# Kernel tuning notes

Measured on AMD Instinct MI355X. Metric: run time of the kernel, lower is better.

The kernel has to match this reference:

```python
import jax, jax.numpy as jnp
import numpy as np
from jax import lax

T, B = 128, 32
V, H = 50257, 512


def _leaky(x, beta):
    # StateLeaky leaky integrator: mem[t] = beta * mem[t-1] + x[t], mem[-1] = 0.
    # x: [T, B, H], beta: [H] (broadcast per-channel decay)
    def step(mem, xt):
        mem = beta * mem + xt
        return mem, mem
    _, mem = lax.scan(step, jnp.zeros_like(x[0]), x)
    return mem  # [T, B, H]


def setup_inputs() -> dict:
    key = jax.random.key(0)
    ks = jax.random.split(key, 10)
    s_emb = 1.0  # nn.Embedding default init N(0,1)
    lim = 1.0 / np.sqrt(H)  # nn.Linear default U(-1/sqrt(fan_in), 1/sqrt(fan_in))
    return {
        "x": jax.random.randint(ks[0], (T, B), 0, V, dtype=jnp.int64),
        "emb": jax.random.normal(ks[1], (V, H), jnp.float32) * s_emb,
        "pos_emb": jax.random.normal(ks[2], (T, H), jnp.float32) * s_emb,
        "beta1": jnp.full((H,), 0.9, jnp.float32),
        "beta2": jnp.full((H,), 0.9, jnp.float32),
        "beta3": jnp.full((H,), 0.9, jnp.float32),
        "fc2_w": jax.random.uniform(ks[3], (H, H), jnp.float32, -lim, lim),
        "fc2_b": jax.random.uniform(ks[4], (H,), jnp.float32, -lim, lim),
        "fc3_w": jax.random.uniform(ks[5], (H, H), jnp.float32, -lim, lim),
        "fc3_b": jax.random.uniform(ks[6], (H,), jnp.float32, -lim, lim),
        "fco_w": jax.random.uniform(ks[7], (V, H), jnp.float32, -lim, lim),
        "fco_b": jax.random.uniform(ks[8], (V,), jnp.float32, -lim, lim),
    }


def reference(x, emb, pos_emb, beta1, beta2, beta3, fc2_w, fc2_b, fc3_w, fc3_b, fco_w, fco_b):
    # token embed + positional embed (pos broadcast over batch dim)
    h = emb[x] + pos_emb[:, None, :]                      # [T, B, H]
    h = _leaky(h, beta1)                                  # StateLeaky 1
    h = jax.nn.relu(jnp.einsum('tbh,oh->tbo', h, fc2_w) + fc2_b)
    h = _leaky(h, beta2)                                  # StateLeaky 2
    h = jax.nn.relu(jnp.einsum('tbh,oh->tbo', h, fc3_w) + fc3_b)
    h = _leaky(h, beta3)                                  # StateLeaky 3
    out = jnp.einsum('tbh,vh->tbv', h, fco_w) + fco_b     # [T, B, V] logits
    return out
```

## Files before the change

### kernel.cpp

```cpp
#include <hip/hip_runtime.h>

typedef __attribute__((ext_vector_type(8))) short short8;
typedef __attribute__((ext_vector_type(4))) float f32x4;
typedef unsigned short u16;
typedef unsigned int u32;

#define DEVI __device__ __forceinline__

DEVI u16 f2bf(float f) {
    union { float f; u32 u; } v; v.f = f;
    u32 r = v.u + 0x7FFFu + ((v.u >> 16) & 1u);
    return (u16)(r >> 16);
}

__global__ void cvt_bf16_kernel(const float* __restrict__ in, u16* __restrict__ out, int n4) {
    int i = blockIdx.x * blockDim.x + threadIdx.x;
    int stride = gridDim.x * blockDim.x;
    for (; i < n4; i += stride) {
        float4 v = reinterpret_cast<const float4*>(in)[i];
        ushort4 o;
        o.x = f2bf(v.x); o.y = f2bf(v.y); o.z = f2bf(v.z); o.w = f2bf(v.w);
        reinterpret_cast<ushort4*>(out)[i] = o;
    }
}

__global__ __launch_bounds__(64)
void embed_leaky_kernel(const int* __restrict__ x, const float* __restrict__ emb,
                        const float* __restrict__ pos, const float* __restrict__ beta,
                        u16* __restrict__ Aout) {
    __shared__ int xs[128];
    int gtid = blockIdx.x * 64 + threadIdx.x;
    int b = gtid >> 9;
    int h = gtid & 511;
    for (int i = threadIdx.x; i < 128; i += 64) xs[i] = x[i * 32 + b];
    __syncthreads();
    float be = beta[h];
    float mem = 0.f;
    for (int t0 = 0; t0 < 128; t0 += 8) {
        float e[8];
#pragma unroll
        for (int j = 0; j < 8; ++j)
            e[j] = emb[(size_t)xs[t0 + j] * 512 + h] + pos[(t0 + j) * 512 + h];
#pragma unroll
        for (int j = 0; j < 8; ++j) {
            mem = be * mem + e[j];
            Aout[(size_t)((t0 + j) * 32 + b) * 512 + h] = f2bf(mem);
        }
    }
}

__global__ __launch_bounds__(64)
void leaky_bf16_kernel(const float* __restrict__ in, const float* __restrict__ beta,
                       u16* __restrict__ Aout) {
    int gtid = blockIdx.x * 64 + threadIdx.x;
    int b = gtid >> 9;
    int h = gtid & 511;
    float be = beta[h];
    float mem = 0.f;
    for (int t0 = 0; t0 < 128; t0 += 8) {
        float v[8];
#pragma unroll
        for (int j = 0; j < 8; ++j)
            v[j] = in[(size_t)((t0 + j) * 32 + b) * 512 + h];
#pragma unroll
        for (int j = 0; j < 8; ++j) {
            mem = be * mem + v[j];
            Aout[(size_t)((t0 + j) * 32 + b) * 512 + h] = f2bf(mem);
        }
    }
}

template<bool RELU>
__global__ __launch_bounds__(256)
void gemm_bt_128(const u16* __restrict__ A, const u16* __restrict__ B,
                 const float* __restrict__ bias, float* __restrict__ C,
                 int M, int N, int K, int tiles_n) {
    __shared__ alignas(16) char smem[32 * 132 * 4];
    u16* As = (u16*)smem;
    u16* Bs = (u16*)(smem + 8192);
    float* Ep = (float*)smem;

    const int tid = threadIdx.x;
    int bm = blockIdx.x / tiles_n;
    int bn = blockIdx.x % tiles_n;
    const int wv = tid >> 6;
    const int lane = tid & 63;
    const int wr = wv >> 1, wc = wv & 1;
    const int lrow = lane & 15;
    const int kg = lane >> 4;
    const int kgp = kg ^ ((lrow >> 1) & 3);

    f32x4 acc[4][4];
#pragma unroll
    for (int i = 0; i < 4; ++i)
#pragma unroll
        for (int j = 0; j < 4; ++j) acc[i][j] = (f32x4){0.f, 0.f, 0.f, 0.f};

    const size_t rowb = (size_t)K * 2;
    const char* Ab = (const char*)A + (size_t)(bm * 128) * rowb;
    const char* Bb = (const char*)B + (size_t)(bn * 128) * rowb;

    float bv[4];
#pragma unroll
    for (int ni = 0; ni < 4; ++ni)
        bv[ni] = bias[bn * 128 + wc * 64 + ni * 16 + lrow];

    for (int k0 = 0; k0 < K; k0 += 32) {
        int k2 = k0 << 1;
#pragma unroll
        for (int r = 0; r < 2; ++r) {
            int s = r * 256 + tid;
            int row = s >> 2;
            int k16g = (s & 3) ^ ((row >> 1) & 3);
            size_t goff = (size_t)row * rowb + k2 + k16g * 16;
            __builtin_amdgcn_global_load_lds(
                (const __attribute__((address_space(1))) void*)(Ab + goff),
                (__attribute__((address_space(3))) void*)((char*)As + s * 16), 16, 0, 0);
            __builtin_amdgcn_global_load_lds(
                (const __attribute__((address_space(1))) void*)(Bb + goff),
                (__attribute__((address_space(3))) void*)((char*)Bs + s * 16), 16, 0, 0);
        }
        __syncthreads();

        short8 a[4], b[4];
#pragma unroll
        for (int mi = 0; mi < 4; ++mi)
            a[mi] = *(const short8*)&As[(wr * 64 + mi * 16 + lrow) * 32 + kgp * 8];
#pragma unroll
        for (int ni = 0; ni < 4; ++ni)
            b[ni] = *(const short8*)&Bs[(wc * 64 + ni * 16 + lrow) * 32 + kgp * 8];
#pragma unroll
        for (int mi = 0; mi < 4; ++mi)
#pragma unroll
            for (int ni = 0; ni < 4; ++ni)
                acc[mi][ni] = __builtin_amdgcn_mfma_f32_16x16x32_bf16(a[mi], b[ni], acc[mi][ni], 0, 0, 0);
        __syncthreads();
    }

#pragma unroll
    for (int mi = 0; mi < 4; ++mi) {
#pragma unroll
        for (int ni = 0; ni < 4; ++ni) {
            int c = wc * 64 + ni * 16 + lrow;
            f32x4 v = acc[mi][ni];
#pragma unroll
            for (int j = 0; j < 4; ++j) {
                float o = v[j] + bv[ni];
                if (RELU) o = fmaxf(o, 0.f);
                Ep[(wr * 16 + kg * 4 + j) * 132 + c] = o;
            }
        }
        __syncthreads();
#pragma unroll
        for (int rr = 0; rr < 8; ++rr) {
            int rl = wv * 8 + rr;
            int grow = bm * 128 + (rl >> 4) * 64 + mi * 16 + (rl & 15);
            size_t base = (size_t)grow * N + bn * 128;
#pragma unroll
            for (int hh = 0; hh < 2; ++hh) {
                int c = hh * 64 + lane;
                C[base + c] = Ep[rl * 132 + c];
            }
        }
        if (mi < 3) __syncthreads();
    }
}

__global__ __launch_bounds__(512, 2)
void gemm_bt_256(const u16* __restrict__ A, const u16* __restrict__ B,
                 const float* __restrict__ bias, float* __restrict__ C,
                 int M, int N, int K, int tiles_m, int tiles_n) {
    extern __shared__ char smem[];
    float* Ep = (float*)smem;

    const int tid = threadIdx.x;
    int nwg = tiles_m * tiles_n;
    int q = nwg >> 3, r = nwg & 7;
    int xcd = blockIdx.x & 7, idx = blockIdx.x >> 3;
    int wg = (xcd < r ? xcd * (q + 1) : r * (q + 1) + (xcd - r) * q) + idx;
    int bn = wg / tiles_m;
    int bm = wg % tiles_m;

    const int wv = tid >> 6;
    const int lane = tid & 63;
    const int wr = wv >> 2;
    const int wc = wv & 3;
    const int lrow = lane & 15;
    const int kg = lane >> 4;

    f32x4 acc[8][4];
#pragma unroll
    for (int i = 0; i < 8; ++i)
#pragma unroll
        for (int j = 0; j < 4; ++j) acc[i][j] = (f32x4){0.f, 0.f, 0.f, 0.f};

    const size_t rowb = (size_t)K * 2;
    const char* Ab = (const char*)A + (size_t)(bm * 256) * rowb;
    const char* Bb = (const char*)B + (size_t)(bn * 256) * rowb;

    float bv[4];
#pragma unroll
    for (int ni = 0; ni < 4; ++ni) {
        int col = bn * 256 + wc * 64 + ni * 16 + lrow;
        bv[ni] = (col < N) ? bias[col] : 0.f;
    }

    auto STAGE = [&](int bufi, int kk) {
        char* dA = smem + bufi * 65536;
        char* dB = dA + 32768;
        int k2 = kk << 1;
#pragma unroll
        for (int i = 0; i < 4; ++i) {
            int s = i * 512 + tid;
            int row = s >> 3;
            int sp = s & 7;
            size_t goff = (size_t)row * rowb + k2 + ((sp ^ (row & 7)) << 4);
            __builtin_amdgcn_global_load_lds(
                (const __attribute__((address_space(1))) void*)(Ab + goff),
                (__attribute__((address_space(3))) void*)(dA + s * 16), 16, 0, 0);
            __builtin_amdgcn_global_load_lds(
                (const __attribute__((address_space(1))) void*)(Bb + goff),
                (__attribute__((address_space(3))) void*)(dB + s * 16), 16, 0, 0);
        }
    };

    const int nt = K >> 6;
    STAGE(0, 0);
    __syncthreads();

    for (int t = 0; t < nt; ++t) {
        const int cur = t & 1;
        const char* As = smem + cur * 65536;
        const char* Bs = As + 32768;

        if (t + 1 < nt) STAGE(cur ^ 1, (t + 1) << 6);

#pragma unroll
        for (int ks = 0; ks < 2; ++ks) {
            short8 a[8], b[4];
#pragma unroll
            for (int mi = 0; mi < 8; ++mi) {
                int rr = wr * 128 + mi * 16 + lrow;
                int sl = (ks * 4 + kg) ^ (rr & 7);
                a[mi] = *(const short8*)(As + rr * 128 + sl * 16);
            }
#pragma unroll
            for (int ni = 0; ni < 4; ++ni) {
                int rr = wc * 64 + ni * 16 + lrow;
                int sl = (ks * 4 + kg) ^ (rr & 7);
                b[ni] = *(const short8*)(Bs + rr * 128 + sl * 16);
            }
#pragma unroll
            for (int mi = 0; mi < 8; ++mi)
#pragma unroll
                for (int ni = 0; ni < 4; ++ni)
                    acc[mi][ni] = __builtin_amdgcn_mfma_f32_16x16x32_bf16(a[mi], b[ni], acc[mi][ni], 0, 0, 0);
        }
        __syncthreads();
    }

#pragma unroll
    for (int ch = 0; ch < 4; ++ch) {
        if (wr == (ch >> 1)) {
            int mibase = (ch & 1) * 4;
#pragma unroll
            for (int m2 = 0; m2 < 4; ++m2) {
#pragma unroll
                for (int ni = 0; ni < 4; ++ni) {
                    int c = wc * 64 + ni * 16 + lrow;
                    f32x4 v = acc[mibase + m2][ni];
#pragma unroll
                    for (int j = 0; j < 4; ++j)
                        Ep[(m2 * 16 + kg * 4 + j) * 260 + c] = v[j] + bv[ni];
                }
            }
        }
        __syncthreads();
#pragma unroll
        for (int rr = 0; rr < 8; ++rr) {
            int rl = wv * 8 + rr;
            int grow = bm * 256 + ch * 64 + rl;
            int gc0 = bn * 256 + lane * 4;
            f32x4 v = *(const f32x4*)&Ep[rl * 260 + lane * 4];
            if (gc0 + 3 < N) {
                __builtin_nontemporal_store(v, (f32x4*)&C[(size_t)grow * N + gc0]);
            } else {
#pragma unroll
                for (int e = 0; e < 4; ++e)
                    if (gc0 + e < N)
                        __builtin_nontemporal_store(v[e], &C[(size_t)grow * N + gc0 + e]);
            }
        }
        if (ch < 3) __syncthreads();
    }
}

extern "C" void kernel_launch(void* const* d_in, const int* in_sizes, int n_in,
                              void* d_out, int out_size, void* d_ws, size_t ws_size,
                              hipStream_t stream) {
    const int* x    = (const int*)d_in[0];
    const float* emb = (const float*)d_in[1];
    const float* pos = (const float*)d_in[2];
    const float* b1 = (const float*)d_in[3];
    const float* b2 = (const float*)d_in[4];
    const float* b3 = (const float*)d_in[5];
    const float* w2 = (const float*)d_in[6];
    const float* fb2 = (const float*)d_in[7];
    const float* w3 = (const float*)d_in[8];
    const float* fb3 = (const float*)d_in[9];
    const float* wo = (const float*)d_in[10];
    const float* fbo = (const float*)d_in[11];
    float* out = (float*)d_out;

    const int V = 50257;
    const int TN = 197;
    const int Vpad = TN * 256;

    static bool lds_cap_set = false;
    if (!lds_cap_set) {
        hipFuncSetAttribute((const void*)gemm_bt_256,
                            hipFuncAttributeMaxDynamicSharedMemorySize, 131072);
        lds_cap_set = true;
    }

    char* p = (char*)d_ws;
    u16* WO = (u16*)p;  p += (size_t)Vpad * 512 * 2;
    u16* W2 = (u16*)p;  p += (size_t)512 * 512 * 2;
    u16* W3 = (u16*)p;  p += (size_t)512 * 512 * 2;
    u16* Abf = (u16*)p; p += (size_t)4096 * 512 * 2;
    float* Hb = (float*)p;

    cvt_bf16_kernel<<<dim3(2048), dim3(256), 0, stream>>>(wo, WO, V * 512 / 4);
    cvt_bf16_kernel<<<dim3(256), dim3(256), 0, stream>>>(w2, W2, 512 * 512 / 4);
    cvt_bf16_kernel<<<dim3(256), dim3(256), 0, stream>>>(w3, W3, 512 * 512 / 4);

    embed_leaky_kernel<<<dim3(256), dim3(64), 0, stream>>>(x, emb, pos, b1, Abf);

    gemm_bt_128<true><<<dim3(32 * 4), dim3(256), 0, stream>>>(Abf, W2, fb2, Hb, 4096, 512, 512, 4);
    leaky_bf16_kernel<<<dim3(256), dim3(64), 0, stream>>>(Hb, b2, Abf);
    gemm_bt_128<true><<<dim3(32 * 4), dim3(256), 0, stream>>>(Abf, W3, fb3, Hb, 4096, 512, 512, 4);
    leaky_bf16_kernel<<<dim3(256), dim3(64), 0, stream>>>(Hb, b3, Abf);
    gemm_bt_256<<<dim3(16 * TN), dim3(512), 131072, stream>>>(Abf, WO, fbo, out, 4096, V, 512, 16, TN);
}
```

Measured before the change: 423.6 us.

## Split K-tile staging into halves with finer-grained vmcnt waits and MFMA priority

Restructures the GEMM main loop so each 64-wide K tile is loaded and consumed in two 32-wide halves, each stored in its own 64-byte-row LDS layout. The old full __syncthreads is replaced with partial s_waitcnt vmcnt plus raw barriers, so the next half-tile load can be issued while the current half computes. It also drops the XOR swizzle and raises wave priority around the MFMA block. The unswizzled 64-byte rows risk LDS bank conflicts on the fragment reads, and the hand-counted vmcnt values must match the number of outstanding loads exactly.

```diff
diff --git a/kernel.cpp b/kernel.cpp
--- a/kernel.cpp
+++ b/kernel.cpp
@@ -205,59 +205,82 @@
         bv[ni] = (col < N) ? bias[col] : 0.f;
     }
 
-    auto STAGE = [&](int bufi, int kk) {
-        char* dA = smem + bufi * 65536;
+    auto STAGE_H = [&](int bufi, int kk, int h) {
+        char* dA = smem + bufi * 65536 + h * 16384;
         char* dB = dA + 32768;
-        int k2 = kk << 1;
-#pragma unroll
-        for (int i = 0; i < 4; ++i) {
-            int s = i * 512 + tid;
-            int row = s >> 3;
-            int sp = s & 7;
-            size_t goff = (size_t)row * rowb + k2 + ((sp ^ (row & 7)) << 4);
+        int kbyte = (kk << 1) + (h << 6);
+#pragma unroll
+        for (int j = 0; j < 2; ++j) {
+            int s = j * 512 + tid;
+            int row = s >> 2;
+            int ls = s & 3;
             __builtin_amdgcn_global_load_lds(
-                (const __attribute__((address_space(1))) void*)(Ab + goff),
+                (const __attribute__((address_space(1))) void*)(Ab + (size_t)row * rowb + kbyte + ls * 16),
                 (__attribute__((address_space(3))) void*)(dA + s * 16), 16, 0, 0);
+        }
+#pragma unroll
+        for (int j = 0; j < 2; ++j) {
+            int s = j * 512 + tid;
+            int row = s >> 2;
+            int ls = s & 3;
             __builtin_amdgcn_global_load_lds(
-                (const __attribute__((address_space(1))) void*)(Bb + goff),
+                (const __attribute__((address_space(1))) void*)(Bb + (size_t)row * rowb + kbyte + ls * 16),
                 (__attribute__((address_space(3))) void*)(dB + s * 16), 16, 0, 0);
         }
     };
 
+    auto COMPUTE = [&](int bufi, int ks) {
+        const char* Ah = smem + bufi * 65536 + ks * 16384;
+        const char* Bh = Ah + 32768;
+        short8 a[8], b[4];
+#pragma unroll
+        for (int mi = 0; mi < 8; ++mi) {
+            int rr = wr * 128 + mi * 16 + lrow;
+            a[mi] = *(const short8*)(Ah + rr * 64 + kg * 16);
+        }
+#pragma unroll
+        for (int ni = 0; ni < 4; ++ni) {
+            int rr = wc * 64 + ni * 16 + lrow;
+            b[ni] = *(const short8*)(Bh + rr * 64 + kg * 16);
+        }
+        __builtin_amdgcn_s_setprio(1);
+#pragma unroll
+        for (int mi = 0; mi < 8; ++mi)
+#pragma unroll
+            for (int ni = 0; ni < 4; ++ni)
+                acc[mi][ni] = __builtin_amdgcn_mfma_f32_16x16x32_bf16(a[mi], b[ni], acc[mi][ni], 0, 0, 0);
+        __builtin_amdgcn_s_setprio(0);
+    };
+
     const int nt = K >> 6;
-    STAGE(0, 0);
+    STAGE_H(0, 0, 0);
+    STAGE_H(0, 0, 1);
+
+    for (int t = 0; t < nt - 1; ++t) {
+        const int c = t & 1;
+        asm volatile("s_waitcnt vmcnt(4)" ::: "memory");
+        __builtin_amdgcn_s_barrier();
+        __builtin_amdgcn_sched_barrier(0);
+        STAGE_H(c ^ 1, (t + 1) << 6, 0);
+        COMPUTE(c, 0);
+        asm volatile("s_waitcnt vmcnt(4)" ::: "memory");
+        __builtin_amdgcn_s_barrier();
+        __builtin_amdgcn_sched_barrier(0);
+        STAGE_H(c ^ 1, (t + 1) << 6, 1);
+        COMPUTE(c, 1);
+    }
+    {
+        const int c = (nt - 1) & 1;
+        asm volatile("s_waitcnt vmcnt(4)" ::: "memory");
+        __builtin_amdgcn_s_barrier();
+        __builtin_amdgcn_sched_barrier(0);
+        COMPUTE(c, 0);
+        asm volatile("s_waitcnt vmcnt(0)" ::: "memory");
+        __builtin_amdgcn_s_barrier();
+        __builtin_amdgcn_sched_barrier(0);
+        COMPUTE(c, 1);
+    }
     __syncthreads();
-
-    for (int t = 0; t < nt; ++t) {
-        const int cur = t & 1;
-        const char* As = smem + cur * 65536;
-        const char* Bs = As + 32768;
-
-        if (t + 1 < nt) STAGE(cur ^ 1, (t + 1) << 6);
-
-#pragma unroll
-        for (int ks = 0; ks < 2; ++ks) {
-            short8 a[8], b[4];
-#pragma unroll
-            for (int mi = 0; mi < 8; ++mi) {
-                int rr = wr * 128 + mi * 16 + lrow;
-                int sl = (ks * 4 + kg) ^ (rr & 7);
-                a[mi] = *(const short8*)(As + rr * 128 + sl * 16);
-            }
-#pragma unroll
-            for (int ni = 0; ni < 4; ++ni) {
-                int rr = wc * 64 + ni * 16 + lrow;
-                int sl = (ks * 4 + kg) ^ (rr & 7);
-                b[ni] = *(const short8*)(Bs + rr * 128 + sl * 16);
-            }
-#pragma unroll
-            for (int mi = 0; mi < 8; ++mi)
-#pragma unroll
-                for (int ni = 0; ni < 4; ++ni)
-                    acc[mi][ni] = __builtin_amdgcn_mfma_f32_16x16x32_bf16(a[mi], b[ni], acc[mi][ni], 0, 0, 0);
-        }
-        __syncthreads();
-    }
 
 #pragma unroll
     for (int ch = 0; ch < 4; ++ch) {
```

New measurement: 434.0 us. 1.02x slower.

## Shrink output GEMM tile to 128x256 with triple-buffered K=32 pipeline

Applied to the files above, without the earlier changes.

Replaces the 256x256 output-projection GEMM with a 128x256 tile using a three-stage LDS ring of K=32 slices, explicit vmcnt waits, single barriers per step and raised MFMA priority. LDS use drops enough to allow up to four workgroups per CU, which is meant to raise occupancy and overlap loads with compute. The three weight conversion launches are also merged into one kernel. The cost is lower per-tile reuse, twice as many workgroups, and an unswizzled LDS layout with 64-byte rows that may cause bank conflicts.

```diff
diff --git a/kernel.cpp b/kernel.cpp
--- a/kernel.cpp
+++ b/kernel.cpp
@@ -13,14 +13,20 @@
     return (u16)(r >> 16);
 }
 
-__global__ void cvt_bf16_kernel(const float* __restrict__ in, u16* __restrict__ out, int n4) {
-    int i = blockIdx.x * blockDim.x + threadIdx.x;
+__global__ void cvt3_kernel(const float* __restrict__ a, u16* __restrict__ oa, int na4,
+                            const float* __restrict__ b, u16* __restrict__ ob, int nb4,
+                            const float* __restrict__ c, u16* __restrict__ oc, int nc4) {
+    int total = na4 + nb4 + nc4;
     int stride = gridDim.x * blockDim.x;
-    for (; i < n4; i += stride) {
-        float4 v = reinterpret_cast<const float4*>(in)[i];
+    for (int i = blockIdx.x * blockDim.x + threadIdx.x; i < total; i += stride) {
+        const float* in; u16* out; int j = i;
+        if (j < na4) { in = a; out = oa; }
+        else if ((j -= na4) < nb4) { in = b; out = ob; }
+        else { j -= nb4; in = c; out = oc; }
+        float4 v = reinterpret_cast<const float4*>(in)[j];
         ushort4 o;
         o.x = f2bf(v.x); o.y = f2bf(v.y); o.z = f2bf(v.z); o.w = f2bf(v.w);
-        reinterpret_cast<ushort4*>(out)[i] = o;
+        reinterpret_cast<ushort4*>(out)[j] = o;
     }
 }
 
@@ -166,10 +172,10 @@
     }
 }
 
-__global__ __launch_bounds__(512, 2)
-void gemm_bt_256(const u16* __restrict__ A, const u16* __restrict__ B,
-                 const float* __restrict__ bias, float* __restrict__ C,
-                 int M, int N, int K, int tiles_m, int tiles_n) {
+__global__ __launch_bounds__(512, 4)
+void gemm_bt_v(const u16* __restrict__ A, const u16* __restrict__ B,
+               const float* __restrict__ bias, float* __restrict__ C,
+               int M, int N, int K, int tiles_m, int tiles_n) {
     extern __shared__ char smem[];
     float* Ep = (float*)smem;
 
@@ -188,15 +194,72 @@
     const int lrow = lane & 15;
     const int kg = lane >> 4;
 
-    f32x4 acc[8][4];
-#pragma unroll
-    for (int i = 0; i < 8; ++i)
+    f32x4 acc[4][4];
+#pragma unroll
+    for (int i = 0; i < 4; ++i)
 #pragma unroll
         for (int j = 0; j < 4; ++j) acc[i][j] = (f32x4){0.f, 0.f, 0.f, 0.f};
 
     const size_t rowb = (size_t)K * 2;
-    const char* Ab = (const char*)A + (size_t)(bm * 256) * rowb;
+    const char* Ab = (const char*)A + (size_t)(bm * 128) * rowb;
     const char* Bb = (const char*)B + (size_t)(bn * 256) * rowb;
+
+    auto STAGE = [&](int bufi, int kk) {
+        char* dA = smem + bufi * 24576;
+        char* dB = dA + 8192;
+        int k2 = kk << 1;
+        {
+            int s = tid;
+            int row = s >> 2, ls = s & 3;
+            __builtin_amdgcn_global_load_lds(
+                (const __attribute__((address_space(1))) void*)(Ab + (size_t)row * rowb + k2 + ls * 16),
+                (__attribute__((address_space(3))) void*)(dA + s * 16), 16, 0, 0);
+        }
+#pragma unroll
+        for (int j = 0; j < 2; ++j) {
+            int s = j * 512 + tid;
+            int row = s >> 2, ls = s & 3;
+            __builtin_amdgcn_global_load_lds(
+                (const __attribute__((address_space(1))) void*)(Bb + (size_t)row * rowb + k2 + ls * 16),
+                (__attribute__((address_space(3))) void*)(dB + s * 16), 16, 0, 0);
+        }
+    };
+
+    auto COMPUTE = [&](int bufi) {
+        const char* Ah = smem + bufi * 24576;
+        const char* Bh = Ah + 8192;
+        short8 a[4], b[4];
+#pragma unroll
+        for (int mi = 0; mi < 4; ++mi) {
+            int rr = wr * 64 + mi * 16 + lrow;
+            a[mi] = *(const short8*)(Ah + rr * 64 + kg * 16);
+        }
+#pragma unroll
+        for (int ni = 0; ni < 4; ++ni) {
+            int rr = wc * 64 + ni * 16 + lrow;
+            b[ni] = *(const short8*)(Bh + rr * 64 + kg * 16);
+        }
+        __builtin_amdgcn_s_setprio(1);
+#pragma unroll
+        for (int mi = 0; mi < 4; ++mi)
+#pragma unroll
+            for (int ni = 0; ni < 4; ++ni)
+                acc[mi][ni] = __builtin_amdgcn_mfma_f32_16x16x32_bf16(a[mi], b[ni], acc[mi][ni], 0, 0, 0);
+        __builtin_amdgcn_s_setprio(0);
+    };
+
+    const int nt = K >> 5;
+    STAGE(0, 0);
+    STAGE(1, 32);
+
+    for (int t = 0; t < nt; ++t) {
+        if (t < nt - 1) asm volatile("s_waitcnt vmcnt(3)" ::: "memory");
+        else            asm volatile("s_waitcnt vmcnt(0)" ::: "memory");
+        __builtin_amdgcn_s_barrier();
+        __builtin_amdgcn_sched_barrier(0);
+        if (t + 2 < nt) STAGE((t + 2) % 3, (t + 2) << 5);
+        COMPUTE(t % 3);
+    }
 
     float bv[4];
 #pragma unroll
@@ -204,71 +267,18 @@
         int col = bn * 256 + wc * 64 + ni * 16 + lrow;
         bv[ni] = (col < N) ? bias[col] : 0.f;
     }
-
-    auto STAGE = [&](int bufi, int kk) {
-        char* dA = smem + bufi * 65536;
-        char* dB = dA + 32768;
-        int k2 = kk << 1;
-#pragma unroll
-        for (int i = 0; i < 4; ++i) {
-            int s = i * 512 + tid;
-            int row = s >> 3;
-            int sp = s & 7;
-            size_t goff = (size_t)row * rowb + k2 + ((sp ^ (row & 7)) << 4);
-            __builtin_amdgcn_global_load_lds(
-                (const __attribute__((address_space(1))) void*)(Ab + goff),
-                (__attribute__((address_space(3))) void*)(dA + s * 16), 16, 0, 0);
-            __builtin_amdgcn_global_load_lds(
-                (const __attribute__((address_space(1))) void*)(Bb + goff),
-                (__attribute__((address_space(3))) void*)(dB + s * 16), 16, 0, 0);
-        }
-    };
-
-    const int nt = K >> 6;
-    STAGE(0, 0);
     __syncthreads();
-
-    for (int t = 0; t < nt; ++t) {
-        const int cur = t & 1;
-        const char* As = smem + cur * 65536;
-        const char* Bs = As + 32768;
-
-        if (t + 1 < nt) STAGE(cur ^ 1, (t + 1) << 6);
-
-#pragma unroll
-        for (int ks = 0; ks < 2; ++ks) {
-            short8 a[8], b[4];
-#pragma unroll
-            for (int mi = 0; mi < 8; ++mi) {
-                int rr = wr * 128 + mi * 16 + lrow;
-                int sl = (ks * 4 + kg) ^ (rr & 7);
-                a[mi] = *(const short8*)(As + rr * 128 + sl * 16);
-            }
-#pragma unroll
-            for (int ni = 0; ni < 4; ++ni) {
-                int rr = wc * 64 + ni * 16 + lrow;
-                int sl = (ks * 4 + kg) ^ (rr & 7);
-                b[ni] = *(const short8*)(Bs + rr * 128 + sl * 16);
-            }
-#pragma unroll
-            for (int mi = 0; mi < 8; ++mi)
-#pragma unroll
-                for (int ni = 0; ni < 4; ++ni)
-                    acc[mi][ni] = __builtin_amdgcn_mfma_f32_16x16x32_bf16(a[mi], b[ni], acc[mi][ni], 0, 0, 0);
-        }
-        __syncthreads();
-    }
 
 #pragma unroll
     for (int ch = 0; ch < 4; ++ch) {
         if (wr == (ch >> 1)) {
-            int mibase = (ch & 1) * 4;
-#pragma unroll
-            for (int m2 = 0; m2 < 4; ++m2) {
+#pragma unroll
+            for (int m2 = 0; m2 < 2; ++m2) {
+                int mi = (ch & 1) * 2 + m2;
 #pragma unroll
                 for (int ni = 0; ni < 4; ++ni) {
                     int c = wc * 64 + ni * 16 + lrow;
-                    f32x4 v = acc[mibase + m2][ni];
+                    f32x4 v = acc[mi][ni];
 #pragma unroll
                     for (int j = 0; j < 4; ++j)
                         Ep[(m2 * 16 + kg * 4 + j) * 260 + c] = v[j] + bv[ni];
@@ -277,9 +287,9 @@
         }
         __syncthreads();
 #pragma unroll
-        for (int rr = 0; rr < 8; ++rr) {
-            int rl = wv * 8 + rr;
-            int grow = bm * 256 + ch * 64 + rl;
+        for (int rr = 0; rr < 4; ++rr) {
+            int rl = wv * 4 + rr;
+            int grow = bm * 128 + ch * 32 + rl;
             int gc0 = bn * 256 + lane * 4;
             f32x4 v = *(const f32x4*)&Ep[rl * 260 + lane * 4];
             if (gc0 + 3 < N) {
@@ -318,8 +328,8 @@
 
     static bool lds_cap_set = false;
     if (!lds_cap_set) {
-        hipFuncSetAttribute((const void*)gemm_bt_256,
-                            hipFuncAttributeMaxDynamicSharedMemorySize, 131072);
+        hipFuncSetAttribute((const void*)gemm_bt_v,
+                            hipFuncAttributeMaxDynamicSharedMemorySize, 73728);
         lds_cap_set = true;
     }
 
@@ -330,9 +340,8 @@
     u16* Abf = (u16*)p; p += (size_t)4096 * 512 * 2;
     float* Hb = (float*)p;
 
-    cvt_bf16_kernel<<<dim3(2048), dim3(256), 0, stream>>>(wo, WO, V * 512 / 4);
-    cvt_bf16_kernel<<<dim3(256), dim3(256), 0, stream>>>(w2, W2, 512 * 512 / 4);
-    cvt_bf16_kernel<<<dim3(256), dim3(256), 0, stream>>>(w3, W3, 512 * 512 / 4);
+    cvt3_kernel<<<dim3(2048), dim3(256), 0, stream>>>(
+        wo, WO, V * 512 / 4, w2, W2, 512 * 512 / 4, w3, W3, 512 * 512 / 4);
 
     embed_leaky_kernel<<<dim3(256), dim3(64), 0, stream>>>(x, emb, pos, b1, Abf);
 
@@ -340,5 +349,5 @@
     leaky_bf16_kernel<<<dim3(256), dim3(64), 0, stream>>>(Hb, b2, Abf);
     gemm_bt_128<true><<<dim3(32 * 4), dim3(256), 0, stream>>>(Abf, W3, fb3, Hb, 4096, 512, 512, 4);
     leaky_bf16_kernel<<<dim3(256), dim3(64), 0, stream>>>(Hb, b3, Abf);
-    gemm_bt_256<<<dim3(16 * TN), dim3(512), 131072, stream>>>(Abf, WO, fbo, out, 4096, V, 512, 16, TN);
-}
+    gemm_bt_v<<<dim3(32 * TN), dim3(512), 73728, stream>>>(Abf, WO, fbo, out, 4096, V, 512, 32, TN);
+}
```

Result: faster. 402.5 us (-5.0%).
